# Optimization experiments

Hardware: AMD Instinct MI355X
Metric: run time of the kernel (lower is better)

Reference implementation:

```python
import jax, jax.numpy as jnp
import numpy as np

IN_FEATURES = 48
OUT_FEATURES = 64
ALPHA = 0.2  # LeakyReLU negative slope
NUM_INTENT = 16
N = 8192


def setup_inputs() -> dict:
    key = jax.random.key(0)
    k1, k2, k3, k4, k5 = jax.random.split(key, 5)
    # Xavier-uniform-ish params (exact init doesn't matter for correctness testing)
    W = jax.random.uniform(k1, (IN_FEATURES, OUT_FEATURES), jnp.float32, -0.3, 0.3)
    a = jax.random.uniform(k2, (2 * OUT_FEATURES, 1), jnp.float32, -0.3, 0.3)
    intent_interaction = jax.random.normal(k3, (NUM_INTENT, NUM_INTENT), jnp.float32) * 0.1
    intent_alpha = jnp.asarray(0.1, jnp.float32)
    inp = jax.random.normal(k4, (N, IN_FEATURES), jnp.float32)
    adj = jnp.ones((N, N), jnp.float32)  # unused by the math, kept for signature fidelity
    intent_labels = jax.random.randint(k5, (N,), 0, NUM_INTENT, jnp.int64 if jax.config.jax_enable_x64 else jnp.int32)
    return {"input": inp, "adj": adj, "W": W, "a": a,
            "intent_interaction": intent_interaction, "intent_alpha": intent_alpha,
            "intent_labels": intent_labels}


def reference(input, adj, W, a, intent_interaction, intent_alpha, intent_labels):
    h = input @ W                       # [N, F]
    F_ = h.shape[1]
    a1 = a[:F_, 0]                      # source part of attention vector
    a2 = a[F_:, 0]                      # target part
    # e[i,j] = leakyrelu(a1.h_i + a2.h_j) without materializing [N,N,2F]
    s1 = h @ a1                         # [N]
    s2 = h @ a2                         # [N]
    spatial_e = jax.nn.leaky_relu(s1[:, None] + s2[None, :], negative_slope=ALPHA)
    # intent bias: gather from interaction matrix, no python loops
    idx = jnp.clip(intent_labels - 1, 0, NUM_INTENT - 1)
    intent_bias = intent_interaction[idx[:, None], idx[None, :]]  # [N, N]
    total_e = spatial_e + intent_alpha * intent_bias
    # NOTE: original softmaxes over dim=0 (columns) and does NOT mask with adj
    attention = jax.nn.softmax(total_e, axis=0)
    h_prime = attention @ h             # [N, F]
    return jax.nn.elu(h_prime)          # concat=True path
```

## Files before the change

kernel.cpp:

```cpp
#include <hip/hip_runtime.h>
#include <hip/hip_bf16.h>

#define NN 8192
#define FF 64
#define INF 48
#define NP 8704
#define NCH (NP/32)
#define LOG2E 1.4426950408889634f

typedef __attribute__((ext_vector_type(8))) short short8;
typedef __attribute__((ext_vector_type(4))) float f32x4;

__device__ __forceinline__ float fexp2(float x) { return __builtin_amdgcn_exp2f(x); }

__device__ __forceinline__ unsigned int packbf2(float a, float b) {
  union { __hip_bfloat162 h2; unsigned int u; } c;
  c.h2 = __float22bfloat162_rn(float2{a, b});
  return c.u;
}
__device__ __forceinline__ unsigned short packbf1(float a) {
  union { __hip_bfloat16 h; unsigned short u; } c;
  c.h = __float2bfloat16(a);
  return c.u;
}

__global__ __launch_bounds__(256) void kZ(float4* __restrict__ U4,
                                          float* __restrict__ s1p, float* __restrict__ s2p,
                                          int* __restrict__ perm, float* __restrict__ Dp,
                                          int* __restrict__ clsc) {
  int idx = blockIdx.x * 256 + threadIdx.x;
  U4[idx] = float4{0.f, 0.f, 0.f, 0.f};
  if (idx < NP) { s1p[idx] = -100.f; s2p[idx] = -100.f; perm[idx] = -1; Dp[idx] = 0.f; }
  if (idx < NCH) clsc[idx] = 0;
}

__global__ __launch_bounds__(256) void kA(const float* __restrict__ in,
                                          const float* __restrict__ W,
                                          const float* __restrict__ a,
                                          const int* __restrict__ labels,
                                          float* __restrict__ h,
                                          float* __restrict__ s1,
                                          float* __restrict__ s2,
                                          int* __restrict__ ci) {
  __shared__ float sIn[4][INF];
  int t = threadIdx.x;
  int w = t >> 6, lane = t & 63;
  int i = blockIdx.x * 4 + w;
  if (lane < INF) sIn[w][lane] = in[i * INF + lane];
  __syncthreads();
  float acc = 0.f;
#pragma unroll
  for (int k = 0; k < INF; k++) acc += sIn[w][k] * W[k * FF + lane];
  h[i * FF + lane] = acc;
  float v1 = acc * a[lane];
  float v2 = acc * a[FF + lane];
#pragma unroll
  for (int off = 32; off > 0; off >>= 1) {
    v1 += __shfl_xor(v1, off, 64);
    v2 += __shfl_xor(v2, off, 64);
  }
  if (lane == 0) {
    s1[i] = v1 * LOG2E;
    s2[i] = v2 * LOG2E;
    int c = labels[i] - 1;
    ci[i] = c < 0 ? 0 : (c > 15 ? 15 : c);
  }
}

__global__ __launch_bounds__(1024) void kSort(const float* __restrict__ s1,
                                              const float* __restrict__ s2,
                                              const int* __restrict__ ci,
                                              int* __restrict__ perm,
                                              float* __restrict__ s1p,
                                              float* __restrict__ s2p,
                                              int* __restrict__ clsc) {
  __shared__ int wcnt[16][16];
  __shared__ int wbase[16][16];
  __shared__ int tot[16];
  __shared__ int cbase[16];
  int t = threadIdx.x;
  int wv = t >> 6, lane = t & 63;
  unsigned long long lower = (1ULL << lane) - 1;
  int c[8], myoff[8];
  float v1[8], v2[8];
#pragma unroll
  for (int k = 0; k < 8; k++) {
    int i = wv * 512 + k * 64 + lane;
    c[k] = ci[i];
    v1[k] = s1[i];
    v2[k] = s2[i];
  }
#pragma unroll 1
  for (int cls = 0; cls < 16; cls++) {
    int run = 0;
#pragma unroll
    for (int k = 0; k < 8; k++) {
      unsigned long long m = __ballot(c[k] == cls);
      if (c[k] == cls) myoff[k] = run + __popcll(m & lower);
      run += __popcll(m);
    }
    if (lane == 0) wcnt[wv][cls] = run;
  }
  __syncthreads();
  if (t < 16) {
    int s = 0;
    for (int w = 0; w < 16; w++) { wbase[w][t] = s; s += wcnt[w][t]; }
    tot[t] = s;
  }
  __syncthreads();
  if (t == 0) {
    int s = 0;
    for (int cls = 0; cls < 16; cls++) { cbase[cls] = s; s += (tot[cls] + 31) & ~31; }
  }
  __syncthreads();
#pragma unroll
  for (int k = 0; k < 8; k++) {
    int i = wv * 512 + k * 64 + lane;
    int pos = cbase[c[k]] + wbase[wv][c[k]] + myoff[k];
    perm[pos] = i;
    s1p[pos] = v1[k];
    s2p[pos] = v2[k];
    clsc[pos >> 5] = c[k];
  }
}

__global__ __launch_bounds__(256) void kD(const float* __restrict__ s1p,
                                          const float* __restrict__ s2p,
                                          const int* __restrict__ clsc,
                                          const float* __restrict__ Bmat,
                                          const float* __restrict__ alpha_p,
                                          float* __restrict__ Dp) {
  __shared__ float EBT[256];
  __shared__ float s1s[512];
  __shared__ int clscs[16];
  int t = threadIdx.x;
  int rs = blockIdx.y;
  EBT[t] = __expf(alpha_p[0] * Bmat[t]);
  s1s[t] = s1p[rs * 512 + t];
  s1s[256 + t] = s1p[rs * 512 + 256 + t];
  if (t < 16) clscs[t] = clsc[rs * 16 + t];
  __syncthreads();
  int jp = blockIdx.x * 512 + t * 2;
  float s2a = s2p[jp], s2b = s2p[jp + 1];
  int cj = clsc[jp >> 5];
  float acc0 = 0.f, acc1 = 0.f;
#pragma unroll 1
  for (int cc = 0; cc < 16; cc++) {
    float w = EBT[clscs[cc] * 16 + cj];
    float p0 = 0.f, p1 = 0.f;
#pragma unroll
    for (int r = 0; r < 32; r++) {
      float sv = s1s[cc * 32 + r];
      float x0 = sv + s2a, x1 = sv + s2b;
      p0 += fexp2(fmaxf(x0, 0.2f * x0));
      p1 += fexp2(fmaxf(x1, 0.2f * x1));
    }
    acc0 = fmaf(p0, w, acc0);
    acc1 = fmaf(p1, w, acc1);
  }
  atomicAdd(&Dp[jp], acc0);
  atomicAdd(&Dp[jp + 1], acc1);
}

__global__ __launch_bounds__(256) void kE(const float* __restrict__ h,
                                          const float* __restrict__ Dp,
                                          const int* __restrict__ perm,
                                          unsigned short* __restrict__ h2T) {
  int t = threadIdx.x;
  int jp = blockIdx.x * 256 + t;
  int fq = blockIdx.y;
  int p = perm[jp];
  if (p < 0) {
#pragma unroll
    for (int k = 0; k < 4; k++) h2T[(size_t)(fq * 4 + k) * NP + jp] = 0;
  } else {
    float g = 1.0f / Dp[jp];
    float4 hv = *(const float4*)&h[p * FF + fq * 4];
    h2T[(size_t)(fq * 4 + 0) * NP + jp] = packbf1(g * hv.x);
    h2T[(size_t)(fq * 4 + 1) * NP + jp] = packbf1(g * hv.y);
    h2T[(size_t)(fq * 4 + 2) * NP + jp] = packbf1(g * hv.z);
    h2T[(size_t)(fq * 4 + 3) * NP + jp] = packbf1(g * hv.w);
  }
}

__global__ __launch_bounds__(256) void kF(const float* __restrict__ s1,
                                          const int* __restrict__ ci,
                                          const float* __restrict__ s2p,
                                          const int* __restrict__ clsc,
                                          const unsigned short* __restrict__ h2T,
                                          const float* __restrict__ Bmat,
                                          const float* __restrict__ alpha_p,
                                          float* __restrict__ U) {
  __shared__ float EBT2[256];
  int t = threadIdx.x;
  int wave = t >> 6, lane = t & 63;
  int quad = lane >> 4, l16 = lane & 15;
  EBT2[t] = __expf(alpha_p[0] * Bmat[(t & 15) * 16 + (t >> 4)]);
  int row0 = blockIdx.x * 64 + wave * 16;
  float s1v = s1[row0 + l16];
  int civ = ci[row0 + l16];
  __syncthreads();

  f32x4 acc0 = {0.f, 0.f, 0.f, 0.f};
  f32x4 acc1 = {0.f, 0.f, 0.f, 0.f};
  f32x4 acc2 = {0.f, 0.f, 0.f, 0.f};
  f32x4 acc3 = {0.f, 0.f, 0.f, 0.f};

  int jbeg = blockIdx.y * (NP / 8);
  int jend = jbeg + (NP / 8);
  for (int j0 = jbeg; j0 < jend; j0 += 32) {
    int cch = clsc[j0 >> 5];
    float w = EBT2[cch * 16 + civ];
    float4 sa = *(const float4*)&s2p[j0 + quad * 8];
    float4 sb = *(const float4*)&s2p[j0 + quad * 8 + 4];
    float e0, e1, e2, e3, e4, e5, e6, e7, x;
    x = s1v + sa.x; e0 = fexp2(fmaxf(x, 0.2f * x)) * w;
    x = s1v + sa.y; e1 = fexp2(fmaxf(x, 0.2f * x)) * w;
    x = s1v + sa.z; e2 = fexp2(fmaxf(x, 0.2f * x)) * w;
    x = s1v + sa.w; e3 = fexp2(fmaxf(x, 0.2f * x)) * w;
    x = s1v + sb.x; e4 = fexp2(fmaxf(x, 0.2f * x)) * w;
    x = s1v + sb.y; e5 = fexp2(fmaxf(x, 0.2f * x)) * w;
    x = s1v + sb.z; e6 = fexp2(fmaxf(x, 0.2f * x)) * w;
    x = s1v + sb.w; e7 = fexp2(fmaxf(x, 0.2f * x)) * w;
    union { short8 s; unsigned int u[4]; } af;
    af.u[0] = packbf2(e0, e1);
    af.u[1] = packbf2(e2, e3);
    af.u[2] = packbf2(e4, e5);
    af.u[3] = packbf2(e6, e7);
    const unsigned short* bbase = h2T + (size_t)l16 * NP + j0 + quad * 8;
    short8 b0 = *(const short8*)(bbase);
    short8 b1 = *(const short8*)(bbase + 16 * NP);
    short8 b2 = *(const short8*)(bbase + 32 * NP);
    short8 b3 = *(const short8*)(bbase + 48 * NP);
    acc0 = __builtin_amdgcn_mfma_f32_16x16x32_bf16(af.s, b0, acc0, 0, 0, 0);
    acc1 = __builtin_amdgcn_mfma_f32_16x16x32_bf16(af.s, b1, acc1, 0, 0, 0);
    acc2 = __builtin_amdgcn_mfma_f32_16x16x32_bf16(af.s, b2, acc2, 0, 0, 0);
    acc3 = __builtin_amdgcn_mfma_f32_16x16x32_bf16(af.s, b3, acc3, 0, 0, 0);
  }
#pragma unroll
  for (int reg = 0; reg < 4; reg++) {
    int ro = (row0 + quad * 4 + reg) * FF + l16;
    atomicAdd(&U[ro + 0], acc0[reg]);
    atomicAdd(&U[ro + 16], acc1[reg]);
    atomicAdd(&U[ro + 32], acc2[reg]);
    atomicAdd(&U[ro + 48], acc3[reg]);
  }
}

__global__ __launch_bounds__(256) void kG(const float* __restrict__ U, float* __restrict__ out) {
  int idx = blockIdx.x * 256 + threadIdx.x;
  float4 v = ((const float4*)U)[idx];
  v.x = v.x > 0.f ? v.x : __expf(v.x) - 1.f;
  v.y = v.y > 0.f ? v.y : __expf(v.y) - 1.f;
  v.z = v.z > 0.f ? v.z : __expf(v.z) - 1.f;
  v.w = v.w > 0.f ? v.w : __expf(v.w) - 1.f;
  ((float4*)out)[idx] = v;
}

extern "C" void kernel_launch(void* const* d_in, const int* in_sizes, int n_in,
                              void* d_out, int out_size, void* d_ws, size_t ws_size,
                              hipStream_t stream) {
  const float* in = (const float*)d_in[0];
  const float* W = (const float*)d_in[2];
  const float* a = (const float*)d_in[3];
  const float* Bmat = (const float*)d_in[4];
  const float* alpha = (const float*)d_in[5];
  const int* labels = (const int*)d_in[6];
  float* out = (float*)d_out;

  float* ws = (float*)d_ws;
  float* h = ws;
  float* U = h + 524288;
  float* s1 = U + 524288;
  float* s2 = s1 + 8192;
  int* ci = (int*)(s2 + 8192);
  float* s1p = (float*)(ci + 8192);
  float* s2p = s1p + NP;
  float* Dp = s2p + NP;
  int* perm = (int*)(Dp + NP);
  int* clsc = perm + NP;
  int* pad = clsc + NCH;
  unsigned short* h2T = (unsigned short*)(pad + 32);

  kZ<<<512, 256, 0, stream>>>((float4*)U, s1p, s2p, perm, Dp, clsc);
  kA<<<2048, 256, 0, stream>>>(in, W, a, labels, h, s1, s2, ci);
  kSort<<<1, 1024, 0, stream>>>(s1, s2, ci, perm, s1p, s2p, clsc);
  kD<<<dim3(17, 17), 256, 0, stream>>>(s1p, s2p, clsc, Bmat, alpha, Dp);
  kE<<<dim3(34, 16), 256, 0, stream>>>(h, Dp, perm, h2T);
  kF<<<dim3(128, 8), 256, 0, stream>>>(s1, ci, s2p, clsc, h2T, Bmat, alpha, U);
  kG<<<512, 256, 0, stream>>>(U, out);
}
```

Baseline: 431.1 us.

## Fuse kernels, drop zero-init and atomics via in-block reductions

Removes the zero-init kernel by having the sort kernel write the padding entries itself. Fuses the column-sum kernel with the scaled transpose kernel, one block per 32-column chunk reducing in shared memory. The main MFMA kernel now splits the j-range across waves in a single block and reduces through LDS, then applies ELU directly. This drops the float atomics and the separate ELU pass, and cuts launches from seven to four, at the cost of less parallelism per launch (272 blocks for kDE, 512 blocks of 16 rows for kF2).

After: 427.5 us. Within noise of the previous version (-0.8%).

```diff
diff --git a/kernel.cpp b/kernel.cpp
--- a/kernel.cpp
+++ b/kernel.cpp
@@ -23,16 +23,7 @@
   c.h = __float2bfloat16(a);
   return c.u;
 }
-
-__global__ __launch_bounds__(256) void kZ(float4* __restrict__ U4,
-                                          float* __restrict__ s1p, float* __restrict__ s2p,
-                                          int* __restrict__ perm, float* __restrict__ Dp,
-                                          int* __restrict__ clsc) {
-  int idx = blockIdx.x * 256 + threadIdx.x;
-  U4[idx] = float4{0.f, 0.f, 0.f, 0.f};
-  if (idx < NP) { s1p[idx] = -100.f; s2p[idx] = -100.f; perm[idx] = -1; Dp[idx] = 0.f; }
-  if (idx < NCH) clsc[idx] = 0;
-}
+__device__ __forceinline__ float elu(float v) { return v > 0.f ? v : __expf(v) - 1.f; }
 
 __global__ __launch_bounds__(256) void kA(const float* __restrict__ in,
                                           const float* __restrict__ W,
@@ -77,7 +68,7 @@
   __shared__ int wcnt[16][16];
   __shared__ int wbase[16][16];
   __shared__ int tot[16];
-  __shared__ int cbase[16];
+  __shared__ int cbase[17];
   int t = threadIdx.x;
   int wv = t >> 6, lane = t & 63;
   unsigned long long lower = (1ULL << lane) - 1;
@@ -111,6 +102,7 @@
   if (t == 0) {
     int s = 0;
     for (int cls = 0; cls < 16; cls++) { cbase[cls] = s; s += (tot[cls] + 31) & ~31; }
+    cbase[16] = s;
   }
   __syncthreads();
 #pragma unroll
@@ -122,81 +114,114 @@
     s2p[pos] = v2[k];
     clsc[pos >> 5] = c[k];
   }
-}
-
-__global__ __launch_bounds__(256) void kD(const float* __restrict__ s1p,
-                                          const float* __restrict__ s2p,
-                                          const int* __restrict__ clsc,
-                                          const float* __restrict__ Bmat,
-                                          const float* __restrict__ alpha_p,
-                                          float* __restrict__ Dp) {
+  int S = cbase[16];
+#pragma unroll 1
+  for (int cls = 0; cls < 16; cls++) {
+    int start = cbase[cls] + tot[cls];
+    int end = (cls < 15) ? cbase[cls + 1] : S;
+    if (t < end - start) {
+      int pos = start + t;
+      perm[pos] = -1;
+      s1p[pos] = -100.f;
+      s2p[pos] = -100.f;
+      clsc[pos >> 5] = cls;
+    }
+  }
+  if (S + t < NP) {
+    int pos = S + t;
+    perm[pos] = -1;
+    s1p[pos] = -100.f;
+    s2p[pos] = -100.f;
+  }
+  if (t < NCH - (S >> 5)) clsc[(S >> 5) + t] = 0;
+}
+
+__global__ __launch_bounds__(256) void kDE(const float* __restrict__ s1p,
+                                           const float* __restrict__ s2p,
+                                           const int* __restrict__ clsc,
+                                           const float* __restrict__ h,
+                                           const int* __restrict__ perm,
+                                           const float* __restrict__ Bmat,
+                                           const float* __restrict__ alpha_p,
+                                           unsigned short* __restrict__ h2T) {
   __shared__ float EBT[256];
-  __shared__ float s1s[512];
-  __shared__ int clscs[16];
+  __shared__ int clsL[NCH];
+  __shared__ float red[8][33];
+  __shared__ float Dinv[32];
+  __shared__ int permL[32];
   int t = threadIdx.x;
-  int rs = blockIdx.y;
+  int blk = blockIdx.x;
+  int jp0 = blk * 32;
   EBT[t] = __expf(alpha_p[0] * Bmat[t]);
-  s1s[t] = s1p[rs * 512 + t];
-  s1s[256 + t] = s1p[rs * 512 + 256 + t];
-  if (t < 16) clscs[t] = clsc[rs * 16 + t];
-  __syncthreads();
-  int jp = blockIdx.x * 512 + t * 2;
-  float s2a = s2p[jp], s2b = s2p[jp + 1];
-  int cj = clsc[jp >> 5];
-  float acc0 = 0.f, acc1 = 0.f;
+  clsL[t] = clsc[t];
+  if (t < NCH - 256) clsL[256 + t] = clsc[256 + t];
+  if (t < 32) permL[t] = perm[jp0 + t];
+  __syncthreads();
+  int c = t & 31, rseg = t >> 5;
+  float s2j = s2p[jp0 + c];
+  int cj = clsL[blk];
+  float acc = 0.f;
 #pragma unroll 1
-  for (int cc = 0; cc < 16; cc++) {
-    float w = EBT[clscs[cc] * 16 + cj];
-    float p0 = 0.f, p1 = 0.f;
-#pragma unroll
-    for (int r = 0; r < 32; r++) {
-      float sv = s1s[cc * 32 + r];
-      float x0 = sv + s2a, x1 = sv + s2b;
-      p0 += fexp2(fmaxf(x0, 0.2f * x0));
-      p1 += fexp2(fmaxf(x1, 0.2f * x1));
-    }
-    acc0 = fmaf(p0, w, acc0);
-    acc1 = fmaf(p1, w, acc1);
-  }
-  atomicAdd(&Dp[jp], acc0);
-  atomicAdd(&Dp[jp + 1], acc1);
-}
-
-__global__ __launch_bounds__(256) void kE(const float* __restrict__ h,
-                                          const float* __restrict__ Dp,
-                                          const int* __restrict__ perm,
-                                          unsigned short* __restrict__ h2T) {
+  for (int ch = 0; ch < 34; ch++) {
+    int chunk = rseg * 34 + ch;
+    float w = EBT[clsL[chunk] * 16 + cj];
+    int base = chunk * 32;
+    float p = 0.f;
+#pragma unroll
+    for (int q = 0; q < 8; q++) {
+      float4 sv = *(const float4*)&s1p[base + q * 4];
+      float x0 = sv.x + s2j, x1 = sv.y + s2j, x2 = sv.z + s2j, x3 = sv.w + s2j;
+      p += fexp2(fmaxf(x0, 0.2f * x0));
+      p += fexp2(fmaxf(x1, 0.2f * x1));
+      p += fexp2(fmaxf(x2, 0.2f * x2));
+      p += fexp2(fmaxf(x3, 0.2f * x3));
+    }
+    acc = fmaf(p, w, acc);
+  }
+  red[rseg][c] = acc;
+  __syncthreads();
+  if (t < 32) {
+    float s = 0.f;
+#pragma unroll
+    for (int r = 0; r < 8; r++) s += red[r][t];
+    Dinv[t] = 1.0f / s;
+  }
+  __syncthreads();
+  int p = permL[c];
+  int fb = rseg * 8;
+  if (p < 0) {
+#pragma unroll
+    for (int k = 0; k < 8; k++) h2T[(size_t)(fb + k) * NP + jp0 + c] = 0;
+  } else {
+    float g = Dinv[c];
+    float4 h0 = *(const float4*)&h[p * FF + fb];
+    float4 h1 = *(const float4*)&h[p * FF + fb + 4];
+    h2T[(size_t)(fb + 0) * NP + jp0 + c] = packbf1(g * h0.x);
+    h2T[(size_t)(fb + 1) * NP + jp0 + c] = packbf1(g * h0.y);
+    h2T[(size_t)(fb + 2) * NP + jp0 + c] = packbf1(g * h0.z);
+    h2T[(size_t)(fb + 3) * NP + jp0 + c] = packbf1(g * h0.w);
+    h2T[(size_t)(fb + 4) * NP + jp0 + c] = packbf1(g * h1.x);
+    h2T[(size_t)(fb + 5) * NP + jp0 + c] = packbf1(g * h1.y);
+    h2T[(size_t)(fb + 6) * NP + jp0 + c] = packbf1(g * h1.z);
+    h2T[(size_t)(fb + 7) * NP + jp0 + c] = packbf1(g * h1.w);
+  }
+}
+
+__global__ __launch_bounds__(256) void kF2(const float* __restrict__ s1,
+                                           const int* __restrict__ ci,
+                                           const float* __restrict__ s2p,
+                                           const int* __restrict__ clsc,
+                                           const unsigned short* __restrict__ h2T,
+                                           const float* __restrict__ Bmat,
+                                           const float* __restrict__ alpha_p,
+                                           float* __restrict__ out) {
+  __shared__ float EBT2[256];
+  __shared__ float red[3 * 1088];
   int t = threadIdx.x;
-  int jp = blockIdx.x * 256 + t;
-  int fq = blockIdx.y;
-  int p = perm[jp];
-  if (p < 0) {
-#pragma unroll
-    for (int k = 0; k < 4; k++) h2T[(size_t)(fq * 4 + k) * NP + jp] = 0;
-  } else {
-    float g = 1.0f / Dp[jp];
-    float4 hv = *(const float4*)&h[p * FF + fq * 4];
-    h2T[(size_t)(fq * 4 + 0) * NP + jp] = packbf1(g * hv.x);
-    h2T[(size_t)(fq * 4 + 1) * NP + jp] = packbf1(g * hv.y);
-    h2T[(size_t)(fq * 4 + 2) * NP + jp] = packbf1(g * hv.z);
-    h2T[(size_t)(fq * 4 + 3) * NP + jp] = packbf1(g * hv.w);
-  }
-}
-
-__global__ __launch_bounds__(256) void kF(const float* __restrict__ s1,
-                                          const int* __restrict__ ci,
-                                          const float* __restrict__ s2p,
-                                          const int* __restrict__ clsc,
-                                          const unsigned short* __restrict__ h2T,
-                                          const float* __restrict__ Bmat,
-                                          const float* __restrict__ alpha_p,
-                                          float* __restrict__ U) {
-  __shared__ float EBT2[256];
-  int t = threadIdx.x;
-  int wave = t >> 6, lane = t & 63;
+  int wv = t >> 6, lane = t & 63;
   int quad = lane >> 4, l16 = lane & 15;
   EBT2[t] = __expf(alpha_p[0] * Bmat[(t & 15) * 16 + (t >> 4)]);
-  int row0 = blockIdx.x * 64 + wave * 16;
+  int row0 = blockIdx.x * 16;
   float s1v = s1[row0 + l16];
   int civ = ci[row0 + l16];
   __syncthreads();
@@ -206,8 +231,8 @@
   f32x4 acc2 = {0.f, 0.f, 0.f, 0.f};
   f32x4 acc3 = {0.f, 0.f, 0.f, 0.f};
 
-  int jbeg = blockIdx.y * (NP / 8);
-  int jend = jbeg + (NP / 8);
+  int jbeg = wv * (NP / 4);
+  int jend = jbeg + (NP / 4);
   for (int j0 = jbeg; j0 < jend; j0 += 32) {
     int cch = clsc[j0 >> 5];
     float w = EBT2[cch * 16 + civ];
@@ -237,24 +262,32 @@
     acc2 = __builtin_amdgcn_mfma_f32_16x16x32_bf16(af.s, b2, acc2, 0, 0, 0);
     acc3 = __builtin_amdgcn_mfma_f32_16x16x32_bf16(af.s, b3, acc3, 0, 0, 0);
   }
-#pragma unroll
-  for (int reg = 0; reg < 4; reg++) {
-    int ro = (row0 + quad * 4 + reg) * FF + l16;
-    atomicAdd(&U[ro + 0], acc0[reg]);
-    atomicAdd(&U[ro + 16], acc1[reg]);
-    atomicAdd(&U[ro + 32], acc2[reg]);
-    atomicAdd(&U[ro + 48], acc3[reg]);
-  }
-}
-
-__global__ __launch_bounds__(256) void kG(const float* __restrict__ U, float* __restrict__ out) {
-  int idx = blockIdx.x * 256 + threadIdx.x;
-  float4 v = ((const float4*)U)[idx];
-  v.x = v.x > 0.f ? v.x : __expf(v.x) - 1.f;
-  v.y = v.y > 0.f ? v.y : __expf(v.y) - 1.f;
-  v.z = v.z > 0.f ? v.z : __expf(v.z) - 1.f;
-  v.w = v.w > 0.f ? v.w : __expf(v.w) - 1.f;
-  ((float4*)out)[idx] = v;
+  if (wv > 0) {
+    int base = (wv - 1) * 1088 + lane * 17;
+#pragma unroll
+    for (int reg = 0; reg < 4; reg++) {
+      red[base + reg] = acc0[reg];
+      red[base + 4 + reg] = acc1[reg];
+      red[base + 8 + reg] = acc2[reg];
+      red[base + 12 + reg] = acc3[reg];
+    }
+  }
+  __syncthreads();
+  if (wv == 0) {
+    int base = lane * 17;
+#pragma unroll
+    for (int reg = 0; reg < 4; reg++) {
+      float v0 = acc0[reg] + red[base + reg] + red[1088 + base + reg] + red[2176 + base + reg];
+      float v1 = acc1[reg] + red[base + 4 + reg] + red[1088 + base + 4 + reg] + red[2176 + base + 4 + reg];
+      float v2 = acc2[reg] + red[base + 8 + reg] + red[1088 + base + 8 + reg] + red[2176 + base + 8 + reg];
+      float v3 = acc3[reg] + red[base + 12 + reg] + red[1088 + base + 12 + reg] + red[2176 + base + 12 + reg];
+      int ro = (row0 + quad * 4 + reg) * FF + l16;
+      out[ro + 0] = elu(v0);
+      out[ro + 16] = elu(v1);
+      out[ro + 32] = elu(v2);
+      out[ro + 48] = elu(v3);
+    }
+  }
 }
 
 extern "C" void kernel_launch(void* const* d_in, const int* in_sizes, int n_in,
@@ -270,23 +303,18 @@
 
   float* ws = (float*)d_ws;
   float* h = ws;
-  float* U = h + 524288;
-  float* s1 = U + 524288;
+  float* s1 = h + 524288;
   float* s2 = s1 + 8192;
   int* ci = (int*)(s2 + 8192);
   float* s1p = (float*)(ci + 8192);
   float* s2p = s1p + NP;
-  float* Dp = s2p + NP;
-  int* perm = (int*)(Dp + NP);
+  int* perm = (int*)(s2p + NP);
   int* clsc = perm + NP;
   int* pad = clsc + NCH;
-  unsigned short* h2T = (unsigned short*)(pad + 32);
-
-  kZ<<<512, 256, 0, stream>>>((float4*)U, s1p, s2p, perm, Dp, clsc);
+  unsigned short* h2T = (unsigned short*)(pad + 16);
+
   kA<<<2048, 256, 0, stream>>>(in, W, a, labels, h, s1, s2, ci);
   kSort<<<1, 1024, 0, stream>>>(s1, s2, ci, perm, s1p, s2p, clsc);
-  kD<<<dim3(17, 17), 256, 0, stream>>>(s1p, s2p, clsc, Bmat, alpha, Dp);
-  kE<<<dim3(34, 16), 256, 0, stream>>>(h, Dp, perm, h2T);
-  kF<<<dim3(128, 8), 256, 0, stream>>>(s1, ci, s2p, clsc, h2T, Bmat, alpha, U);
-  kG<<<512, 256, 0, stream>>>(U, out);
-}
+  kDE<<<NCH, 256, 0, stream>>>(s1p, s2p, clsc, h, perm, Bmat, alpha, h2T);
+  kF2<<<512, 256, 0, stream>>>(s1, ci, s2p, clsc, h2T, Bmat, alpha, out);
+}
```
